# Performance work log

Hardware: AMD Instinct MI355X
Metric: run time of the kernel (lower is better)

Reference implementation:

```python
import jax, jax.numpy as jnp
import numpy as np

N_NODES = 100000
N_EDGES = 600000
HIDDEN = 128


def setup_inputs() -> dict:
    key = jax.random.key(0)
    ks = jax.random.split(key, 5)
    x = jax.random.normal(ks[0], (N_NODES, HIDDEN), dtype=jnp.float32)
    edge_index = jax.random.randint(ks[1], (2, N_EDGES), 0, N_NODES, dtype=jnp.int64)
    edge_weight = jax.random.uniform(ks[2], (N_EDGES,), dtype=jnp.float32)
    # MLP params: Linear(2*H+1 -> H), ReLU, Linear(H -> 1)
    W1 = jax.random.normal(ks[3], (2 * HIDDEN + 1, HIDDEN), dtype=jnp.float32) * (1.0 / np.sqrt(2 * HIDDEN + 1))
    b1 = jnp.zeros((HIDDEN,), dtype=jnp.float32)
    W2 = jax.random.normal(ks[4], (HIDDEN, 1), dtype=jnp.float32) * (1.0 / np.sqrt(HIDDEN))
    b2 = jnp.zeros((1,), dtype=jnp.float32)
    return {"x": x, "edge_index": edge_index, "edge_weight": edge_weight,
            "W1": W1, "b1": b1, "W2": W2, "b2": b2}


def reference(x, edge_index, edge_weight, W1, b1, W2, b2):
    num_nodes = x.shape[0]
    src = edge_index[0]
    tgt = edge_index[1]
    h_src = x[src]                      # [E, H] gather
    h_tgt = x[tgt]                      # [E, H] gather
    w = edge_weight[:, None]            # [E, 1]
    concat = jnp.concatenate([h_src, h_tgt, w], axis=-1)   # [E, 2H+1]
    hidden = jax.nn.relu(concat @ W1 + b1)                 # [E, H]
    scores = (hidden @ W2 + b2)[:, 0]                      # [E]
    # NOTE: the original _softmax_edge's max-pass uses index_put_(accumulate=True)
    # on a -inf buffer, so every touched entry stays -inf and is then replaced by 0;
    # the net effect is NO max subtraction. Faithful math: plain exp / segment_sum.
    exp_scores = jnp.exp(scores)
    sum_exp = jax.ops.segment_sum(exp_scores, tgt, num_segments=num_nodes)
    sum_exp = jnp.maximum(sum_exp, 1e-12)
    alpha = exp_scores / sum_exp[tgt]                      # [E]
    out = jax.ops.segment_sum(alpha[:, None] * h_src, tgt, num_segments=num_nodes)
    return x + out
```

## Files before the change

### kernel.cpp

```cpp
#include <hip/hip_runtime.h>
#include <hip/hip_bf16.h>

#define N_NODES 100000
#define N_EDGES 600000
#define HID 128
#define SCAN_NB 391
#define GEMM_BLOCKS 1563
#define FILL_BLOCKS 586


typedef short bf16x8 __attribute__((ext_vector_type(8)));
typedef float f32x4  __attribute__((ext_vector_type(4)));

__device__ inline unsigned short f2bf(float v) {
    __hip_bfloat16 h = __float2bfloat16(v);
    return *(unsigned short*)&h;
}
__device__ inline unsigned int pack2(float a, float b) {
    return (unsigned int)f2bf(a) | ((unsigned int)f2bf(b) << 16);
}
__device__ inline float2 bfpair(unsigned int u) {
    float lo = __uint_as_float(u << 16);
    float hi = __uint_as_float(u & 0xffff0000u);
    return make_float2(lo, hi);
}
__device__ inline void lds_barrier() {
    asm volatile("s_waitcnt lgkmcnt(0)" ::: "memory");
    __builtin_amdgcn_s_barrier();
}

__global__ __launch_bounds__(256) void k_prep(const float* __restrict__ W1,
                                              unsigned short* __restrict__ Bh,
                                              int* __restrict__ deg)
{
    int idx = blockIdx.x * 256 + threadIdx.x;
    if (idx < N_NODES) deg[idx] = 0;
    if (idx < 32768) {
        int n = idx & 255;
        int k = idx >> 8;
        float v = (n < HID) ? W1[k * HID + n] : W1[(HID + k) * HID + (n - HID)];
        Bh[(k >> 5) * 8192 + n * 32 + (k & 31)] = f2bf(v);
    }
}

__global__ __launch_bounds__(256) void k_count(const int* __restrict__ ei,
                                               int* __restrict__ deg)
{
    int e = blockIdx.x * blockDim.x + threadIdx.x;
    if (e < N_EDGES) atomicAdd(&deg[ei[N_EDGES + e]], 1);
}

__global__ __launch_bounds__(256) void k_rowptr(const int* __restrict__ deg,
                                                int* __restrict__ rowptr,
                                                int* __restrict__ cursor)
{
    __shared__ int s[256];
    int t = threadIdx.x;
    int b = blockIdx.x;
    int lim = b * 256;

    int acc = 0;
    for (int i = t; i < lim; i += 256) acc += deg[i];
    s[t] = acc;
    __syncthreads();
    #pragma unroll
    for (int off = 128; off > 0; off >>= 1) {
        if (t < off) s[t] += s[t + off];
        __syncthreads();
    }
    int pb = s[0];
    __syncthreads();

    int idx = lim + t;
    int v = (idx < N_NODES) ? deg[idx] : 0;
    s[t] = v;
    __syncthreads();
    #pragma unroll
    for (int off = 1; off < 256; off <<= 1) {
        int u = (t >= off) ? s[t - off] : 0;
        __syncthreads();
        s[t] += u;
        __syncthreads();
    }
    if (idx < N_NODES) {
        int r = pb + s[t] - v;
        rowptr[idx] = r;
        cursor[idx] = r;
    }
    if (idx == 0) rowptr[N_NODES] = N_EDGES;
}

__global__ __launch_bounds__(256) void k_gemm_fill(const float* __restrict__ x,
                                                   const unsigned short* __restrict__ BhG,
                                                   unsigned short* __restrict__ zbuf,
                                                   unsigned short* __restrict__ y2buf,
                                                   const int* __restrict__ ei,
                                                   const float* __restrict__ ew,
                                                   int* __restrict__ cursor,
                                                   uint2* __restrict__ eprs)
{
    __shared__ unsigned short Ah[64 * 128];

    if (blockIdx.x >= GEMM_BLOCKS) {
        int fb = blockIdx.x - GEMM_BLOCKS;
        for (int e = fb * 256 + threadIdx.x; e < N_EDGES; e += FILL_BLOCKS * 256) {
            int tgt = ei[N_EDGES + e];
            int pos = atomicAdd(&cursor[tgt], 1);
            eprs[pos] = make_uint2((unsigned int)ei[e], __float_as_uint(ew[e]));
        }
        return;
    }

    const int tid  = threadIdx.x;
    const int bm   = blockIdx.x * 64;
    const int wave = tid >> 6;
    const int lane = tid & 63;
    const int q    = lane >> 4;
    const int ln   = lane & 15;

    {
        const int r  = tid >> 2;
        const int c  = tid & 3;
        const int gm = bm + r;
        const bool ok = gm < N_NODES;
        const float* px = &x[(size_t)gm * HID + c * 32];

        float4 v0 = make_float4(0.f,0.f,0.f,0.f), v1=v0, v2=v0, v3=v0, v4=v0, v5=v0, v6=v0, v7=v0;
        if (ok) {
            v0 = *(const float4*)(px + 0);  v1 = *(const float4*)(px + 4);
            v2 = *(const float4*)(px + 8);  v3 = *(const float4*)(px + 12);
            v4 = *(const float4*)(px + 16); v5 = *(const float4*)(px + 20);
            v6 = *(const float4*)(px + 24); v7 = *(const float4*)(px + 28);
        }
        uint4 ch0, ch1, ch2, ch3;
        ch0.x = pack2(v0.x, v0.y); ch0.y = pack2(v0.z, v0.w); ch0.z = pack2(v1.x, v1.y); ch0.w = pack2(v1.z, v1.w);
        ch1.x = pack2(v2.x, v2.y); ch1.y = pack2(v2.z, v2.w); ch1.z = pack2(v3.x, v3.y); ch1.w = pack2(v3.z, v3.w);
        ch2.x = pack2(v4.x, v4.y); ch2.y = pack2(v4.z, v4.w); ch2.z = pack2(v5.x, v5.y); ch2.w = pack2(v5.z, v5.w);
        ch3.x = pack2(v6.x, v6.y); ch3.y = pack2(v6.z, v6.w); ch3.z = pack2(v7.x, v7.y); ch3.w = pack2(v7.z, v7.w);

        char* rowp = (char*)Ah + r * 256;
        const int swz = (r & 7) << 4;
        *(uint4*)(rowp + ((c * 64 +  0) ^ swz)) = ch0;
        *(uint4*)(rowp + ((c * 64 + 16) ^ swz)) = ch1;
        *(uint4*)(rowp + ((c * 64 + 32) ^ swz)) = ch2;
        *(uint4*)(rowp + ((c * 64 + 48) ^ swz)) = ch3;

        if (ok) {
            unsigned short* zp = &zbuf[(size_t)gm * 256 + 128 + c * 32];
            *(uint4*)(zp + 0)  = ch0;
            *(uint4*)(zp + 8)  = ch1;
            *(uint4*)(zp + 16) = ch2;
            *(uint4*)(zp + 24) = ch3;
        }
    }
    lds_barrier();

    bf16x8 ah[4][4];
    {
        const int swzr = (ln & 7) << 4;
        #pragma unroll
        for (int mt = 0; mt < 4; ++mt) {
            const char* rowp = (const char*)Ah + (mt * 16 + ln) * 256;
            #pragma unroll
            for (int ks = 0; ks < 4; ++ks) {
                ah[mt][ks] = *(const bf16x8*)(rowp + ((ks * 64 + q * 16) ^ swzr));
            }
        }
    }

    f32x4 acc[4][4] = {};
    #pragma unroll
    for (int nt = 0; nt < 4; ++nt) {
        bf16x8 bh[4];
        #pragma unroll
        for (int ks = 0; ks < 4; ++ks) {
            bh[ks] = *(const bf16x8*)&BhG[ks * 8192 + (wave * 64 + nt * 16 + ln) * 32 + q * 8];
        }
        #pragma unroll
        for (int mt = 0; mt < 4; ++mt) {
            #pragma unroll
            for (int ks = 0; ks < 4; ++ks) {
                acc[mt][nt] = __builtin_amdgcn_mfma_f32_16x16x32_bf16(bh[ks], ah[mt][ks], acc[mt][nt], 0, 0, 0);
            }
        }
    }

    #pragma unroll
    for (int mt = 0; mt < 4; ++mt) {
        int node = bm + mt * 16 + ln;
        if (node < N_NODES) {
            #pragma unroll
            for (int nt = 0; nt < 4; ++nt) {
                int col0 = wave * 64 + nt * 16 + q * 4;
                unsigned int lo = pack2(acc[mt][nt][0], acc[mt][nt][1]);
                unsigned int hi = pack2(acc[mt][nt][2], acc[mt][nt][3]);
                if (col0 < 128) *(uint2*)&zbuf[(size_t)node * 256 + col0] = make_uint2(lo, hi);
                else            *(uint2*)&y2buf[(size_t)node * 128 + (col0 - 128)] = make_uint2(lo, hi);
            }
        }
    }
}

__global__ __launch_bounds__(256) void k_fused(const unsigned int* __restrict__ zu,
                                               const unsigned int* __restrict__ y2u,
                                               const int* __restrict__ rowptr,
                                               const uint2* __restrict__ eprs,
                                               const float* __restrict__ x,
                                               const float* __restrict__ W1,
                                               const float* __restrict__ b1,
                                               const float* __restrict__ W2,
                                               const float* __restrict__ b2,
                                               float* __restrict__ out)
{
    int n = (blockIdx.x * blockDim.x + threadIdx.x) >> 6;
    int lane = threadIdx.x & 63;
    if (n >= N_NODES) return;
    int ql = lane & 15;
    int qi = lane >> 4;
    int c0 = ql * 8;

    uint4 uy2 = *(const uint4*)&y2u[(size_t)n * 64 + ql * 4];
    float2 y2a = bfpair(uy2.x), y2b = bfpair(uy2.y), y2c = bfpair(uy2.z), y2d = bfpair(uy2.w);
    float4 bv0 = *(const float4*)&b1[c0];
    float4 bv1 = *(const float4*)&b1[c0 + 4];
    float4 wr0 = *(const float4*)&W1[256 * HID + c0];
    float4 wr1 = *(const float4*)&W1[256 * HID + c0 + 4];
    float4 w20 = *(const float4*)&W2[c0];
    float4 w21 = *(const float4*)&W2[c0 + 4];
    float p0 = y2a.x + bv0.x, p1 = y2a.y + bv0.y, p2 = y2b.x + bv0.z, p3 = y2b.y + bv0.w;
    float p4 = y2c.x + bv1.x, p5 = y2c.y + bv1.y, p6 = y2d.x + bv1.z, p7 = y2d.y + bv1.w;
    float b2v = b2[0];

    int beg = rowptr[n], end = rowptr[n + 1];
    float a0 = 0.f, a1 = 0.f, a2 = 0.f, a3 = 0.f;
    float a4 = 0.f, a5 = 0.f, a6 = 0.f, a7 = 0.f;
    float denom = 0.f;

    for (int i = beg; i < end; i += 8) {
        int idxA = i + qi;
        int idxB = i + 4 + qi;
        bool vA = idxA < end;
        bool vB = idxB < end;
        int ieA = vA ? idxA : (end - 1);
        int ieB = vB ? idxB : (end - 1);
        uint2 epA = eprs[ieA];
        uint2 epB = eprs[ieB];
        size_t baseA = (size_t)epA.x * 128;
        size_t baseB = (size_t)epB.x * 128;
        float wa = __uint_as_float(epA.y);
        float wb = __uint_as_float(epB.y);
        uint4 uyA = *(const uint4*)&zu[baseA + ql * 4];
        uint4 uxA = *(const uint4*)&zu[baseA + 64 + ql * 4];
        uint4 uyB = *(const uint4*)&zu[baseB + ql * 4];
        uint4 uxB = *(const uint4*)&zu[baseB + 64 + ql * 4];

        float2 ya = bfpair(uyA.x), yb = bfpair(uyA.y), yc = bfpair(uyA.z), yd = bfpair(uyA.w);
        float h0 = fmaxf(fmaf(wa, wr0.x, ya.x + p0), 0.f);
        float h1 = fmaxf(fmaf(wa, wr0.y, ya.y + p1), 0.f);
        float h2 = fmaxf(fmaf(wa, wr0.z, yb.x + p2), 0.f);
        float h3 = fmaxf(fmaf(wa, wr0.w, yb.y + p3), 0.f);
        float h4 = fmaxf(fmaf(wa, wr1.x, yc.x + p4), 0.f);
        float h5 = fmaxf(fmaf(wa, wr1.y, yc.y + p5), 0.f);
        float h6 = fmaxf(fmaf(wa, wr1.z, yd.x + p6), 0.f);
        float h7 = fmaxf(fmaf(wa, wr1.w, yd.y + p7), 0.f);
        float sA = ((h0 * w20.x + h1 * w20.y) + (h2 * w20.z + h3 * w20.w))
                 + ((h4 * w21.x + h5 * w21.y) + (h6 * w21.z + h7 * w21.w));

        float2 za = bfpair(uyB.x), zb = bfpair(uyB.y), zc = bfpair(uyB.z), zd = bfpair(uyB.w);
        float g0 = fmaxf(fmaf(wb, wr0.x, za.x + p0), 0.f);
        float g1 = fmaxf(fmaf(wb, wr0.y, za.y + p1), 0.f);
        float g2 = fmaxf(fmaf(wb, wr0.z, zb.x + p2), 0.f);
        float g3 = fmaxf(fmaf(wb, wr0.w, zb.y + p3), 0.f);
        float g4 = fmaxf(fmaf(wb, wr1.x, zc.x + p4), 0.f);
        float g5 = fmaxf(fmaf(wb, wr1.y, zc.y + p5), 0.f);
        float g6 = fmaxf(fmaf(wb, wr1.z, zd.x + p6), 0.f);
        float g7 = fmaxf(fmaf(wb, wr1.w, zd.y + p7), 0.f);
        float sB = ((g0 * w20.x + g1 * w20.y) + (g2 * w20.z + g3 * w20.w))
                 + ((g4 * w21.x + g5 * w21.y) + (g6 * w21.z + g7 * w21.w));

        #pragma unroll
        for (int m = 1; m <= 8; m <<= 1) {
            sA += __shfl_xor(sA, m, 64);
            sB += __shfl_xor(sB, m, 64);
        }
        float esA = vA ? __expf(sA + b2v) : 0.f;
        float esB = vB ? __expf(sB + b2v) : 0.f;

        float2 xa = bfpair(uxA.x), xb = bfpair(uxA.y), xc = bfpair(uxA.z), xd = bfpair(uxA.w);
        float2 ua = bfpair(uxB.x), ub = bfpair(uxB.y), uc = bfpair(uxB.z), ud = bfpair(uxB.w);
        a0 = fmaf(esA, xa.x, fmaf(esB, ua.x, a0));
        a1 = fmaf(esA, xa.y, fmaf(esB, ua.y, a1));
        a2 = fmaf(esA, xb.x, fmaf(esB, ub.x, a2));
        a3 = fmaf(esA, xb.y, fmaf(esB, ub.y, a3));
        a4 = fmaf(esA, xc.x, fmaf(esB, uc.x, a4));
        a5 = fmaf(esA, xc.y, fmaf(esB, uc.y, a5));
        a6 = fmaf(esA, xd.x, fmaf(esB, ud.x, a6));
        a7 = fmaf(esA, xd.y, fmaf(esB, ud.y, a7));
        denom += esA + esB;
    }

    #pragma unroll
    for (int m = 16; m <= 32; m <<= 1) {
        a0 += __shfl_xor(a0, m, 64); a1 += __shfl_xor(a1, m, 64);
        a2 += __shfl_xor(a2, m, 64); a3 += __shfl_xor(a3, m, 64);
        a4 += __shfl_xor(a4, m, 64); a5 += __shfl_xor(a5, m, 64);
        a6 += __shfl_xor(a6, m, 64); a7 += __shfl_xor(a7, m, 64);
        denom += __shfl_xor(denom, m, 64);
    }

    if (qi == 0) {
        float4 xt0 = *(const float4*)&x[(size_t)n * HID + c0];
        float4 xt1 = *(const float4*)&x[(size_t)n * HID + c0 + 4];
        float inv = 1.0f / fmaxf(denom, 1e-12f);
        float4 o0, o1;
        o0.x = xt0.x + a0 * inv; o0.y = xt0.y + a1 * inv;
        o0.z = xt0.z + a2 * inv; o0.w = xt0.w + a3 * inv;
        o1.x = xt1.x + a4 * inv; o1.y = xt1.y + a5 * inv;
        o1.z = xt1.z + a6 * inv; o1.w = xt1.w + a7 * inv;
        *(float4*)&out[(size_t)n * HID + c0]     = o0;
        *(float4*)&out[(size_t)n * HID + c0 + 4] = o1;
    }
}

extern "C" void kernel_launch(void* const* d_in, const int* in_sizes, int n_in,
                              void* d_out, int out_size, void* d_ws, size_t ws_size,
                              hipStream_t stream) {
    const float* x  = (const float*)d_in[0];
    const int*   ei = (const int*)d_in[1];
    const float* ew = (const float*)d_in[2];
    const float* W1 = (const float*)d_in[3];
    const float* b1 = (const float*)d_in[4];
    const float* W2 = (const float*)d_in[5];
    const float* b2 = (const float*)d_in[6];
    float* out = (float*)d_out;
    char* ws = (char*)d_ws;

    const size_t deg_b    = 400000;
    const size_t rowptr_b = 400016;
    const size_t cursor_b = 400000;
    const size_t eprs_b   = 4800000;
    const size_t part_b   = 1568;
    const size_t pb_b     = 1568;
    const size_t Bh_b     = 65536;

    char* p = ws;
    int* deg      = (int*)p;             p += deg_b;
    int* rowptr   = (int*)p;             p += rowptr_b;
    int* cursor   = (int*)p;             p += cursor_b;
    uint2* eprs   = (uint2*)p;           p += eprs_b;
    p += part_b;
    p += pb_b;
    unsigned short* BhG = (unsigned short*)p;  p += Bh_b;
    unsigned short* zbuf  = (unsigned short*)p;  p += (size_t)N_NODES * 256 * 2;
    unsigned short* y2buf = (unsigned short*)p;

    const int edge_blocks = (N_EDGES + 255) / 256;
    const int node_wave_blocks = (N_NODES * 64 + 255) / 256;

    hipLaunchKernelGGL(k_prep,   dim3(SCAN_NB), dim3(256), 0, stream, W1, BhG, deg);
    hipLaunchKernelGGL(k_count,  dim3(edge_blocks), dim3(256), 0, stream, ei, deg);
    hipLaunchKernelGGL(k_rowptr, dim3(SCAN_NB), dim3(256), 0, stream, deg, rowptr, cursor);
    hipLaunchKernelGGL(k_gemm_fill, dim3(GEMM_BLOCKS + FILL_BLOCKS), dim3(256), 0, stream,
                       x, BhG, zbuf, y2buf, ei, ew, cursor, eprs);
    hipLaunchKernelGGL(k_fused,  dim3(node_wave_blocks), dim3(256), 0, stream,
                       (const unsigned int*)zbuf, (const unsigned int*)y2buf,
                       rowptr, eprs, x, W1, b1, W2, b2, out);
}
```

Baseline: 319.6 us.

## Replace cursor atomics in CSR fill with per-edge ranks from counting pass

The counting kernel now records the return value of its degree atomicAdd as a per-edge rank, so the fill step computes each edge's CSR slot as rowptr[tgt]+rank without a second atomic pass. The separate fill blocks are removed and each GEMM block scatters a fixed chunk of 384 edges after its matrix work. This drops 600k contended atomics and the cursor buffer. In exchange it writes and reads a 2.4 MB rank array and puts the scatter on the GEMM blocks' critical path.

```diff
diff --git a/kernel.cpp b/kernel.cpp
--- a/kernel.cpp
+++ b/kernel.cpp
@@ -6,7 +6,7 @@
 #define HID 128
 #define SCAN_NB 391
 #define GEMM_BLOCKS 1563
-#define FILL_BLOCKS 586
+#define EDGES_PER_BLOCK 384
 
 
 typedef short bf16x8 __attribute__((ext_vector_type(8)));
@@ -44,15 +44,15 @@
 }
 
 __global__ __launch_bounds__(256) void k_count(const int* __restrict__ ei,
-                                               int* __restrict__ deg)
+                                               int* __restrict__ deg,
+                                               int* __restrict__ rank)
 {
     int e = blockIdx.x * blockDim.x + threadIdx.x;
-    if (e < N_EDGES) atomicAdd(&deg[ei[N_EDGES + e]], 1);
+    if (e < N_EDGES) rank[e] = atomicAdd(&deg[ei[N_EDGES + e]], 1);
 }
 
 __global__ __launch_bounds__(256) void k_rowptr(const int* __restrict__ deg,
-                                                int* __restrict__ rowptr,
-                                                int* __restrict__ cursor)
+                                                int* __restrict__ rowptr)
 {
     __shared__ int s[256];
     int t = threadIdx.x;
@@ -82,11 +82,7 @@
         s[t] += u;
         __syncthreads();
     }
-    if (idx < N_NODES) {
-        int r = pb + s[t] - v;
-        rowptr[idx] = r;
-        cursor[idx] = r;
-    }
+    if (idx < N_NODES) rowptr[idx] = pb + s[t] - v;
     if (idx == 0) rowptr[N_NODES] = N_EDGES;
 }
 
@@ -96,20 +92,11 @@
                                                    unsigned short* __restrict__ y2buf,
                                                    const int* __restrict__ ei,
                                                    const float* __restrict__ ew,
-                                                   int* __restrict__ cursor,
+                                                   const int* __restrict__ rowptr,
+                                                   const int* __restrict__ rank,
                                                    uint2* __restrict__ eprs)
 {
     __shared__ unsigned short Ah[64 * 128];
-
-    if (blockIdx.x >= GEMM_BLOCKS) {
-        int fb = blockIdx.x - GEMM_BLOCKS;
-        for (int e = fb * 256 + threadIdx.x; e < N_EDGES; e += FILL_BLOCKS * 256) {
-            int tgt = ei[N_EDGES + e];
-            int pos = atomicAdd(&cursor[tgt], 1);
-            eprs[pos] = make_uint2((unsigned int)ei[e], __float_as_uint(ew[e]));
-        }
-        return;
-    }
 
     const int tid  = threadIdx.x;
     const int bm   = blockIdx.x * 64;
@@ -197,6 +184,16 @@
                 if (col0 < 128) *(uint2*)&zbuf[(size_t)node * 256 + col0] = make_uint2(lo, hi);
                 else            *(uint2*)&y2buf[(size_t)node * 128 + (col0 - 128)] = make_uint2(lo, hi);
             }
+        }
+    }
+
+    {
+        int e0 = blockIdx.x * EDGES_PER_BLOCK;
+        int e1 = e0 + EDGES_PER_BLOCK; if (e1 > N_EDGES) e1 = N_EDGES;
+        for (int e = e0 + tid; e < e1; e += 256) {
+            int tgt = ei[N_EDGES + e];
+            int pos = rowptr[tgt] + rank[e];
+            eprs[pos] = make_uint2((unsigned int)ei[e], __float_as_uint(ew[e]));
         }
     }
 }
@@ -337,19 +334,15 @@
 
     const size_t deg_b    = 400000;
     const size_t rowptr_b = 400016;
-    const size_t cursor_b = 400000;
+    const size_t rank_b   = 2400000;
     const size_t eprs_b   = 4800000;
-    const size_t part_b   = 1568;
-    const size_t pb_b     = 1568;
     const size_t Bh_b     = 65536;
 
     char* p = ws;
     int* deg      = (int*)p;             p += deg_b;
     int* rowptr   = (int*)p;             p += rowptr_b;
-    int* cursor   = (int*)p;             p += cursor_b;
+    int* rank     = (int*)p;             p += rank_b;
     uint2* eprs   = (uint2*)p;           p += eprs_b;
-    p += part_b;
-    p += pb_b;
     unsigned short* BhG = (unsigned short*)p;  p += Bh_b;
     unsigned short* zbuf  = (unsigned short*)p;  p += (size_t)N_NODES * 256 * 2;
     unsigned short* y2buf = (unsigned short*)p;
@@ -358,10 +351,10 @@
     const int node_wave_blocks = (N_NODES * 64 + 255) / 256;
 
     hipLaunchKernelGGL(k_prep,   dim3(SCAN_NB), dim3(256), 0, stream, W1, BhG, deg);
-    hipLaunchKernelGGL(k_count,  dim3(edge_blocks), dim3(256), 0, stream, ei, deg);
-    hipLaunchKernelGGL(k_rowptr, dim3(SCAN_NB), dim3(256), 0, stream, deg, rowptr, cursor);
-    hipLaunchKernelGGL(k_gemm_fill, dim3(GEMM_BLOCKS + FILL_BLOCKS), dim3(256), 0, stream,
-                       x, BhG, zbuf, y2buf, ei, ew, cursor, eprs);
+    hipLaunchKernelGGL(k_count,  dim3(edge_blocks), dim3(256), 0, stream, ei, deg, rank);
+    hipLaunchKernelGGL(k_rowptr, dim3(SCAN_NB), dim3(256), 0, stream, deg, rowptr);
+    hipLaunchKernelGGL(k_gemm_fill, dim3(GEMM_BLOCKS), dim3(256), 0, stream,
+                       x, BhG, zbuf, y2buf, ei, ew, rowptr, rank, eprs);
     hipLaunchKernelGGL(k_fused,  dim3(node_wave_blocks), dim3(256), 0, stream,
                        (const unsigned int*)zbuf, (const unsigned int*)y2buf,
                        rowptr, eprs, x, W1, b1, W2, b2, out);
```

After: 317.9 us. Within noise of the previous version (-0.5%).
